# Kernel tuning notes

Hardware: AMD Instinct MI355X
Metric: run time of the kernel (lower is better)

The kernel has to match this reference:

```python
import math
import jax, jax.numpy as jnp
import numpy as np

LOG_NORM = -0.5 * math.log(2.0 * math.pi)  # per-dim gaussian normalizer
HEADS = 4
EM_ITERS = 5


def _mab(x, wq, bq, wk, bk, wv, bv, wo, bo):
    # Set-Transformer SAB(x) = MAB(x, x), ln=False
    B, S, D = x.shape
    dh = D // HEADS
    q = (x @ wq + bq).reshape(B, S, HEADS, dh)
    k = (x @ wk + bk).reshape(B, S, HEADS, dh)
    v = (x @ wv + bv).reshape(B, S, HEADS, dh)
    att = jax.nn.softmax(jnp.einsum('bqhd,bkhd->bhqk', q, k) / math.sqrt(D), axis=-1)
    o = q + jnp.einsum('bhqk,bkhd->bqhd', att, v)
    o = o.reshape(B, S, D)
    return o + jax.nn.relu(o @ wo + bo)


def setup_inputs() -> dict:
    key = jax.random.key(0)
    ks = jax.random.split(key, 16)
    B, S, D, L, K, MC = 16, 256, 512, 64, 20, 10
    s512 = 1.0 / math.sqrt(512.0)
    inp = {
        'H': jax.random.normal(ks[0], (B, S, D), jnp.float32),
        'eps': jax.random.normal(ks[1], (B * S, MC, L), jnp.float32),
        'sab_wq': jax.random.normal(ks[2], (2, D, D), jnp.float32) * s512,
        'sab_bq': jnp.zeros((2, D), jnp.float32),
        'sab_wk': jax.random.normal(ks[3], (2, D, D), jnp.float32) * s512,
        'sab_bk': jnp.zeros((2, D), jnp.float32),
        'sab_wv': jax.random.normal(ks[4], (2, D, D), jnp.float32) * s512,
        'sab_bv': jnp.zeros((2, D), jnp.float32),
        'sab_wo': jax.random.normal(ks[5], (2, D, D), jnp.float32) * s512,
        'sab_bo': jnp.zeros((2, D), jnp.float32),
        'wz': jax.random.normal(ks[6], (D, 2 * L), jnp.float32) * 0.02,
        'bz': jnp.zeros((2 * L,), jnp.float32),
        'w1': jax.random.normal(ks[7], (L, 2 * D), jnp.float32) * (1.0 / math.sqrt(L)),
        'b1': jnp.zeros((2 * D,), jnp.float32),
        'w2': jax.random.normal(ks[8], (2 * D, 2 * D), jnp.float32) * (1.0 / math.sqrt(2 * D)),
        'b2': jnp.zeros((2 * D,), jnp.float32),
        'w3': jax.random.normal(ks[9], (2 * D, D), jnp.float32) * (1.0 / math.sqrt(2 * D)),
        'b3': jnp.zeros((D,), jnp.float32),
    }
    rng = np.random.default_rng(1)
    # component_size distinct indices into the S*MC latent samples, per batch
    inp['init_idx'] = jnp.asarray(
        np.stack([rng.permutation(S * MC)[:K] for _ in range(B)]).astype(np.int32))
    return inp


def reference(H, eps, init_idx, sab_wq, sab_bq, sab_wk, sab_bk, sab_wv, sab_bv,
              sab_wo, sab_bo, wz, bz, w1, b1, w2, b2, w3, b3):
    B, S, D = H.shape
    MC, L = eps.shape[1], eps.shape[2]
    K = init_idx.shape[1]

    # q(z|x): two SABs + linear head
    h = H
    for i in range(2):
        h = _mab(h, sab_wq[i], sab_bq[i], sab_wk[i], sab_bk[i],
                 sab_wv[i], sab_bv[i], sab_wo[i], sab_bo[i])
    stats = h @ wz + bz                                    # [B,S,2L]
    mean, logvar = stats[..., :L], stats[..., L:]
    std = jnp.exp(0.5 * logvar)
    z = mean.reshape(B * S, 1, L) + eps * std.reshape(B * S, 1, L)
    z = z.reshape(B, S, MC, L)
    all_z = z.reshape(B, S * MC, L)                        # [B,N,L]

    # unsupervised EM prior (unit-variance GMM); distances via expansion
    pi = jnp.full((B, K), 1.0 / K, dtype=H.dtype)
    mu = jnp.take_along_axis(all_z, init_idx[:, :, None], axis=1)  # [B,K,L]
    x2 = jnp.sum(all_z * all_z, axis=-1)                   # [B,N]
    for _ in range(EM_ITERS):
        m2 = jnp.sum(mu * mu, axis=-1)                     # [B,K]
        ll = (-0.5 * (x2[:, :, None] - 2.0 * jnp.einsum('bnd,bkd->bnk', all_z, mu)
                      + m2[:, None, :]) + L * LOG_NORM + jnp.log(pi)[:, None, :])
        post = jax.nn.softmax(ll, axis=-1)                 # [B,N,K]
        Nk = post.sum(axis=1)                              # [B,K]
        pi = Nk / Nk.sum(axis=-1, keepdims=True)
        mu = jnp.einsum('bnk,bnd->bkd', post, all_z) / Nk[:, :, None]
    pi = jax.lax.stop_gradient(pi)
    mu = jax.lax.stop_gradient(mu)

    # reconstruction
    zf = z.reshape(-1, L)
    hr = jax.nn.relu(zf @ w1 + b1)
    hr = jax.nn.relu(hr @ w2 + b2)
    hr = jax.nn.relu(hr @ w3 + b3)
    hr = hr.reshape(B, S, MC, D)
    rec_loss = jnp.sum((hr - H[:, :, None, :]) ** 2) / (B * S * MC)

    # KL
    log_qz = jnp.sum(-0.5 * (logvar[:, :, None, :]
                             + (z - mean[:, :, None, :]) ** 2 / jnp.exp(logvar)[:, :, None, :])
                     + LOG_NORM, axis=-1)                  # [B,S,MC]
    z2 = jnp.sum(z * z, axis=-1)                           # [B,S,MC]
    m2 = jnp.sum(mu * mu, axis=-1)                         # [B,K]
    ll = (-0.5 * (z2[..., None] - 2.0 * jnp.einsum('bsmd,bkd->bsmk', z, mu)
                  + m2[:, None, None, :]) + L * LOG_NORM + jnp.log(pi)[:, None, None, :])
    log_pz = jax.scipy.special.logsumexp(ll, axis=-1)      # [B,S,MC]
    kl_loss = jnp.mean(log_qz - log_pz)
    return rec_loss, kl_loss
```

## Files before the change

kernel.cpp:

```cpp
#include <hip/hip_runtime.h>
#include <hip/hip_bf16.h>
#include <math.h>


#define BATCH 16
#define SEQ 256
#define DIM 512
#define NH 4
#define DH 128
#define LD 64
#define KC 20
#define MC 10
#define NPTS 2560
#define BS_TOT 4096
#define NROWS 40960
#define LOG_NORM (-0.9189385332046727f)

typedef __attribute__((ext_vector_type(8))) short bf16x8;
typedef __attribute__((ext_vector_type(4))) float f32x4;
typedef __hip_bfloat16 bf;

__device__ inline float warpReduceSum(float v) {
    for (int o = 32; o > 0; o >>= 1) v += __shfl_down(v, o);
    return v;
}

__device__ inline void async_copy16(const bf* g, bf* l) {
    __builtin_amdgcn_global_load_lds(
        (const __attribute__((address_space(1))) unsigned int*)g,
        (__attribute__((address_space(3))) unsigned int*)l, 16, 0, 0);
}

__device__ inline void split_store(float x, bf* ph, bf* pl, long idx) {
    const bf h = __float2bfloat16(x);
    ph[idx] = h;
    pl[idx] = __float2bfloat16(x - __bfloat162float(h));
}

template<int MODE>
__global__ __launch_bounds__(256, 3)
void gemm3t(const bf* __restrict__ Ah, const bf* __restrict__ Al,
            const bf* __restrict__ Bh, const bf* __restrict__ Bl,
            int K, int lda, int ldb,
            const float* __restrict__ b0, const float* __restrict__ b1v,
            const float* __restrict__ b2v,
            float* __restrict__ outF,
            bf* __restrict__ P1h, bf* __restrict__ P1l,
            bf* __restrict__ P2h, bf* __restrict__ P2l,
            bf* __restrict__ P3h, bf* __restrict__ P3l,
            const bf* __restrict__ Rh, const bf* __restrict__ Rl)
{
    __shared__ __align__(16) char smem[49152];
    float* Xs = (float*)smem;

    const int t = threadIdx.x;
    const int m0 = blockIdx.y * 64, n0 = blockIdx.x * 128;
    const int w = t >> 6, lane = t & 63;
    const int wn = w * 32;
    const int fm = lane & 15, quad = lane >> 4, fk = quad * 8;
    const int srow = t >> 2, scol = (t & 3) * 8;

    f32x4 acc[4][2];
#pragma unroll
    for (int i = 0; i < 4; i++)
#pragma unroll
        for (int j = 0; j < 2; j++) acc[i][j] = (f32x4){0.f, 0.f, 0.f, 0.f};

    const int nk2 = K >> 6;
    for (int kk2 = 0; kk2 < nk2; kk2++) {
#pragma unroll
        for (int h = 0; h < 2; h++) {
            const int kk = kk2 * 2 + h;
            char* base = smem + h * 24576;
            bf* Ash = (bf*)base;
            bf* Asl = (bf*)(base + 4096);
            bf* Bsh = (bf*)(base + 8192);
            bf* Bsl = (bf*)(base + 16384);
            const long ao = (long)(m0 + srow) * lda + kk * 32 + scol;
            const long bo = (long)(n0 + srow) * ldb + kk * 32 + scol;
            async_copy16(Ah + ao, Ash + w * 512);
            async_copy16(Al + ao, Asl + w * 512);
            async_copy16(Bh + bo, Bsh + w * 512);
            async_copy16(Bh + bo + 64L * ldb, Bsh + 2048 + w * 512);
            async_copy16(Bl + bo, Bsl + w * 512);
            async_copy16(Bl + bo + 64L * ldb, Bsl + 2048 + w * 512);
        }
        __syncthreads();

#pragma unroll
        for (int h = 0; h < 2; h++) {
            char* base = smem + h * 24576;
            bf* Ash = (bf*)base;
            bf* Asl = (bf*)(base + 4096);
            bf* Bsh = (bf*)(base + 8192);
            bf* Bsl = (bf*)(base + 16384);
            bf16x8 afh[4], afl[4], bfh[2], bfl[2];
#pragma unroll
            for (int mi = 0; mi < 4; mi++) {
                afh[mi] = *(const bf16x8*)&Ash[(mi * 16 + fm) * 32 + fk];
                afl[mi] = *(const bf16x8*)&Asl[(mi * 16 + fm) * 32 + fk];
            }
#pragma unroll
            for (int ni = 0; ni < 2; ni++) {
                bfh[ni] = *(const bf16x8*)&Bsh[(wn + ni * 16 + fm) * 32 + fk];
                bfl[ni] = *(const bf16x8*)&Bsl[(wn + ni * 16 + fm) * 32 + fk];
            }
#pragma unroll
            for (int mi = 0; mi < 4; mi++)
#pragma unroll
                for (int ni = 0; ni < 2; ni++) {
                    acc[mi][ni] = __builtin_amdgcn_mfma_f32_16x16x32_bf16(
                        afh[mi], bfh[ni], acc[mi][ni], 0, 0, 0);
                    acc[mi][ni] = __builtin_amdgcn_mfma_f32_16x16x32_bf16(
                        afh[mi], bfl[ni], acc[mi][ni], 0, 0, 0);
                    acc[mi][ni] = __builtin_amdgcn_mfma_f32_16x16x32_bf16(
                        afl[mi], bfh[ni], acc[mi][ni], 0, 0, 0);
                }
        }
        __syncthreads();
    }

    const int rl = t >> 2;
    const int cc4 = (t & 3) * 16;

    for (int p = 0; p < 2; p++) {
        if ((w >> 1) == p) {
            const int cb = wn - p * 64;
#pragma unroll
            for (int mi = 0; mi < 4; mi++)
#pragma unroll
                for (int ni = 0; ni < 2; ni++) {
                    const int c = cb + ni * 16 + fm;
#pragma unroll
                    for (int r = 0; r < 4; r++)
                        Xs[(mi * 16 + quad * 4 + r) * 68 + c] = acc[mi][ni][r];
                }
        }
        __syncthreads();

        if (MODE == 0 && n0 >= 1024) {
            const int hh = (n0 >> 7) & 3;
            const int dd = p * 64 + rl;
            const int bb = m0 >> 8;
            const int sb = (m0 & 255) + cc4;
            const float bias = b2v[hh * 128 + dd];
            const long ob = (((long)(bb * NH + hh) * DH + dd) << 8) + sb;
#pragma unroll
            for (int j = 0; j < 2; j++) {
                bf16x8 vh, vl;
#pragma unroll
                for (int i = 0; i < 8; i++) {
                    const float x = Xs[(cc4 + j * 8 + i) * 68 + rl] + bias;
                    const bf h = __float2bfloat16(x);
                    vh[i] = *(const short*)&h;
                    const bf l = __float2bfloat16(x - __bfloat162float(h));
                    vl[i] = *(const short*)&l;
                }
                *(bf16x8*)&P3h[ob + j * 8] = vh;
                *(bf16x8*)&P3l[ob + j * 8] = vl;
            }
        } else {
            float xv[16];
#pragma unroll
            for (int i = 0; i < 4; i++)
                *(float4*)&xv[i * 4] = *(const float4*)&Xs[rl * 68 + cc4 + i * 4];

            if (MODE == 0) {
                const int which = n0 >> 9;
                const int colq = (n0 & 511) + p * 64 + cc4;
                const float* bias = which ? b1v : b0;
                bf* Ph = which ? P2h : P1h;
                bf* Pl = which ? P2l : P1l;
                const long ob = (long)(m0 + rl) * 512 + colq;
#pragma unroll
                for (int j = 0; j < 2; j++) {
                    bf16x8 vh, vl;
#pragma unroll
                    for (int i = 0; i < 8; i++) {
                        const float x = xv[j * 8 + i] + bias[colq + j * 8 + i];
                        const bf h = __float2bfloat16(x); vh[i] = *(const short*)&h;
                        const bf l = __float2bfloat16(x - __bfloat162float(h));
                        vl[i] = *(const short*)&l;
                    }
                    *(bf16x8*)&Ph[ob + j * 8] = vh;
                    *(bf16x8*)&Pl[ob + j * 8] = vl;
                }
            } else if (MODE == 3) {
                const int colg = n0 + p * 64 + cc4;
                const long ob = (long)(m0 + rl) * 512 + colg;
#pragma unroll
                for (int j = 0; j < 2; j++) {
                    const bf16x8 rh = *(const bf16x8*)&Rh[ob + j * 8];
                    const bf16x8 rv = *(const bf16x8*)&Rl[ob + j * 8];
                    bf16x8 vh, vl;
#pragma unroll
                    for (int i = 0; i < 8; i++) {
                        short sh = rh[i], sl = rv[i];
                        float x = fmaxf(xv[j * 8 + i] + b0[colg + j * 8 + i], 0.f)
                                + __bfloat162float(*(const bf*)&sh)
                                + __bfloat162float(*(const bf*)&sl);
                        const bf h = __float2bfloat16(x); vh[i] = *(const short*)&h;
                        const bf l = __float2bfloat16(x - __bfloat162float(h));
                        vl[i] = *(const short*)&l;
                    }
                    *(bf16x8*)&P1h[ob + j * 8] = vh;
                    *(bf16x8*)&P1l[ob + j * 8] = vl;
                }
            } else {
                const int colg = p * 64 + cc4;
                const long ob = (long)(m0 + rl) * 128 + colg;
#pragma unroll
                for (int i = 0; i < 4; i++) {
                    float4 v = *(float4*)&xv[i * 4];
                    v.x += b0[colg + i * 4 + 0];
                    v.y += b0[colg + i * 4 + 1];
                    v.z += b0[colg + i * 4 + 2];
                    v.w += b0[colg + i * 4 + 3];
                    *(float4*)&outF[ob + i * 4] = v;
                }
            }
        }
        __syncthreads();
    }
}

__global__ __launch_bounds__(256)
void attn_fused(const bf* __restrict__ qh, const bf* __restrict__ ql,
                const bf* __restrict__ kh, const bf* __restrict__ kl,
                const bf* __restrict__ vTh, const bf* __restrict__ vTl,
                bf* __restrict__ oh, bf* __restrict__ ol)
{
    __shared__ __align__(16) char smem[43008];
    bf* Qsh = (bf*)smem;            bf* Qsl = (bf*)(smem + 4096);
    bf* Ksh = (bf*)(smem + 8192);   bf* Ksl = (bf*)(smem + 24576);
    bf* Psh = (bf*)smem;            bf* Psl = (bf*)(smem + 4096);
    bf* Vsh = (bf*)(smem + 8192);   bf* Vsl = (bf*)(smem + 16384);
    float (*red)[4]  = (float(*)[4])(smem + 40960);
    float (*red2)[4] = (float(*)[4])(smem + 41984);

    const int t = threadIdx.x;
    const int z = blockIdx.y;
    const int m0 = blockIdx.x * 64;
    const int bb = z >> 2, hh = z & 3;
    const long hOff = (long)bb * 131072 + (long)hh * 128;
    const long vOff = (long)z * 32768;

    const int w = t >> 6, lane = t & 63;
    const int fm = lane & 15;
    const int quad = lane >> 4;
    const int fk = quad * 8;
    const int srow = t >> 2, scol = (t & 3) * 8;

    f32x4 acc[4][4];
#pragma unroll
    for (int i = 0; i < 4; i++)
#pragma unroll
        for (int j = 0; j < 4; j++) acc[i][j] = (f32x4){0.f, 0.f, 0.f, 0.f};

    for (int kk = 0; kk < 4; kk++) {
        const long ao = hOff + (long)(m0 + srow) * 512 + kk * 32 + scol;
        const long bo = hOff + (long)srow * 512 + kk * 32 + scol;
        async_copy16(qh + ao, Qsh + w * 512);
        async_copy16(ql + ao, Qsl + w * 512);
#pragma unroll
        for (int j = 0; j < 4; j++) {
            async_copy16(kh + bo + (long)j * 64 * 512, Ksh + w * 512 + j * 2048);
            async_copy16(kl + bo + (long)j * 64 * 512, Ksl + w * 512 + j * 2048);
        }
        __syncthreads();

        bf16x8 afh[4], afl[4];
#pragma unroll
        for (int mi = 0; mi < 4; mi++) {
            afh[mi] = *(const bf16x8*)&Qsh[(mi * 16 + fm) * 32 + fk];
            afl[mi] = *(const bf16x8*)&Qsl[(mi * 16 + fm) * 32 + fk];
        }
#pragma unroll
        for (int ni = 0; ni < 4; ni++) {
            const bf16x8 bh = *(const bf16x8*)&Ksh[(w * 64 + ni * 16 + fm) * 32 + fk];
            const bf16x8 bl = *(const bf16x8*)&Ksl[(w * 64 + ni * 16 + fm) * 32 + fk];
#pragma unroll
            for (int mi = 0; mi < 4; mi++) {
                acc[mi][ni] = __builtin_amdgcn_mfma_f32_16x16x32_bf16(
                    afh[mi], bh, acc[mi][ni], 0, 0, 0);
                acc[mi][ni] = __builtin_amdgcn_mfma_f32_16x16x32_bf16(
                    afh[mi], bl, acc[mi][ni], 0, 0, 0);
                acc[mi][ni] = __builtin_amdgcn_mfma_f32_16x16x32_bf16(
                    afl[mi], bh, acc[mi][ni], 0, 0, 0);
            }
        }
        __syncthreads();
    }

    const float alpha = 0.044194173824159216f;
#pragma unroll
    for (int mi = 0; mi < 4; mi++)
#pragma unroll
        for (int r = 0; r < 4; r++) {
            float m = -1e30f;
#pragma unroll
            for (int ni = 0; ni < 4; ni++) m = fmaxf(m, acc[mi][ni][r]);
            for (int o = 8; o > 0; o >>= 1) m = fmaxf(m, __shfl_xor(m, o));
            if (fm == 0) red[mi * 16 + quad * 4 + r][w] = m;
        }
    __syncthreads();
    float invr[4][4];
#pragma unroll
    for (int mi = 0; mi < 4; mi++)
#pragma unroll
        for (int r = 0; r < 4; r++) {
            const int rowl = mi * 16 + quad * 4 + r;
            const float mx = fmaxf(fmaxf(red[rowl][0], red[rowl][1]),
                                   fmaxf(red[rowl][2], red[rowl][3]));
            float s = 0.f;
#pragma unroll
            for (int ni = 0; ni < 4; ni++) {
                const float e = __expf((acc[mi][ni][r] - mx) * alpha);
                acc[mi][ni][r] = e;
                s += e;
            }
            for (int o = 8; o > 0; o >>= 1) s += __shfl_xor(s, o);
            if (fm == 0) red2[rowl][w] = s;
        }
    __syncthreads();
#pragma unroll
    for (int mi = 0; mi < 4; mi++)
#pragma unroll
        for (int r = 0; r < 4; r++) {
            const int rowl = mi * 16 + quad * 4 + r;
            invr[mi][r] = 1.f / (red2[rowl][0] + red2[rowl][1] + red2[rowl][2] + red2[rowl][3]);
        }

    f32x4 acc2[4][2];
#pragma unroll
    for (int i = 0; i < 4; i++)
#pragma unroll
        for (int j = 0; j < 2; j++) acc2[i][j] = (f32x4){0.f, 0.f, 0.f, 0.f};

    for (int kc = 0; kc < 8; kc++) {
        if (w == (kc >> 1)) {
            const int nib = (kc & 1) * 2;
#pragma unroll
            for (int mi = 0; mi < 4; mi++)
#pragma unroll
                for (int r = 0; r < 4; r++) {
                    const int row = mi * 16 + quad * 4 + r;
#pragma unroll
                    for (int j = 0; j < 2; j++) {
                        const float p = acc[mi][nib + j][r] * invr[mi][r];
                        const int cc = j * 16 + fm;
                        const bf h = __float2bfloat16(p);
                        Psh[row * 32 + cc] = h;
                        Psl[row * 32 + cc] = __float2bfloat16(p - __bfloat162float(h));
                    }
                }
        }
        const long vo = vOff + (long)srow * 256 + kc * 32 + scol;
        async_copy16(vTh + vo, Vsh + w * 512);
        async_copy16(vTh + vo + 64L * 256, Vsh + w * 512 + 2048);
        async_copy16(vTl + vo, Vsl + w * 512);
        async_copy16(vTl + vo + 64L * 256, Vsl + w * 512 + 2048);
        __syncthreads();

        bf16x8 pfh[4], pfl[4];
#pragma unroll
        for (int mi = 0; mi < 4; mi++) {
            pfh[mi] = *(const bf16x8*)&Psh[(mi * 16 + fm) * 32 + fk];
            pfl[mi] = *(const bf16x8*)&Psl[(mi * 16 + fm) * 32 + fk];
        }
#pragma unroll
        for (int ni = 0; ni < 2; ni++) {
            const bf16x8 vh = *(const bf16x8*)&Vsh[(w * 32 + ni * 16 + fm) * 32 + fk];
            const bf16x8 vl = *(const bf16x8*)&Vsl[(w * 32 + ni * 16 + fm) * 32 + fk];
#pragma unroll
            for (int mi = 0; mi < 4; mi++) {
                acc2[mi][ni] = __builtin_amdgcn_mfma_f32_16x16x32_bf16(
                    pfh[mi], vh, acc2[mi][ni], 0, 0, 0);
                acc2[mi][ni] = __builtin_amdgcn_mfma_f32_16x16x32_bf16(
                    pfh[mi], vl, acc2[mi][ni], 0, 0, 0);
                acc2[mi][ni] = __builtin_amdgcn_mfma_f32_16x16x32_bf16(
                    pfl[mi], vh, acc2[mi][ni], 0, 0, 0);
            }
        }
        __syncthreads();
    }

#pragma unroll
    for (int ni = 0; ni < 2; ni++) {
        const int col = hh * 128 + w * 32 + ni * 16 + fm;
#pragma unroll
        for (int mi = 0; mi < 4; mi++)
#pragma unroll
            for (int r = 0; r < 4; r++) {
                const int row = mi * 16 + quad * 4 + r;
                const long idx = (long)(bb * 256 + m0 + row) * 512 + col;
                const float x = acc2[mi][ni][r]
                    + __bfloat162float(qh[idx]) + __bfloat162float(ql[idx]);
                split_store(x, oh, ol, idx);
            }
    }
}

template<bool SQLOSS>
__global__ __launch_bounds__(256, 4)
void gemm_mfma(const bf* __restrict__ A, const bf* __restrict__ BT,
               bf* __restrict__ C,
               const float* __restrict__ bias,
               const float* __restrict__ Href,
               float* __restrict__ lossAcc,
               int K, int N)
{
    __shared__ __align__(16) char smem[32768];
    bf* Cs  = (bf*)smem;
    __shared__ float redS[4];

    const int t = threadIdx.x;
    const int flat = blockIdx.y * gridDim.x + blockIdx.x;
    const int lane8 = flat & 7;
    const int grp = flat >> 3;
    const int n_blk = grp % gridDim.x;
    const int m_blk = (grp / gridDim.x) * 8 + lane8;
    const int m0 = m_blk * 128, n0 = n_blk * 128;

    const int w = t >> 6, lane = t & 63;
    const int wm = (w >> 1) * 64, wn = (w & 1) * 64;
    const int fm = lane & 15;
    const int quad = lane >> 4;
    const int fk = quad * 8;
    const int srow = t >> 2, scol = (t & 3) * 8;

    f32x4 acc[4][4];
#pragma unroll
    for (int i = 0; i < 4; i++)
#pragma unroll
        for (int j = 0; j < 4; j++) acc[i][j] = (f32x4){0.f, 0.f, 0.f, 0.f};

    const int nk2 = K >> 6;
    for (int kt2 = 0; kt2 < nk2; kt2++) {
#pragma unroll
        for (int h = 0; h < 2; h++) {
            const int kt = kt2 * 2 + h;
            bf* Asg = (bf*)(smem + h * 16384);
            bf* Bsg = (bf*)(smem + h * 16384 + 8192);
            const bf* ga = A + (long)(m0 + srow) * K + kt * 32 + scol;
            const bf* gb = BT + (long)(n0 + srow) * K + kt * 32 + scol;
            async_copy16(ga, Asg + w * 512);
            async_copy16(ga + 64L * K, Asg + 2048 + w * 512);
            async_copy16(gb, Bsg + w * 512);
            async_copy16(gb + 64L * K, Bsg + 2048 + w * 512);
        }
        __syncthreads();

#pragma unroll
        for (int h = 0; h < 2; h++) {
            bf* Asg = (bf*)(smem + h * 16384);
            bf* Bsg = (bf*)(smem + h * 16384 + 8192);
            bf16x8 af[4], bfr[4];
#pragma unroll
            for (int mi = 0; mi < 4; mi++)
                af[mi] = *(const bf16x8*)&Asg[(wm + mi * 16 + fm) * 32 + fk];
#pragma unroll
            for (int ni = 0; ni < 4; ni++)
                bfr[ni] = *(const bf16x8*)&Bsg[(wn + ni * 16 + fm) * 32 + fk];
#pragma unroll
            for (int mi = 0; mi < 4; mi++)
#pragma unroll
                for (int ni = 0; ni < 4; ni++)
                    acc[mi][ni] = __builtin_amdgcn_mfma_f32_16x16x32_bf16(
                        af[mi], bfr[ni], acc[mi][ni], 0, 0, 0);
        }
        __syncthreads();
    }

    if (SQLOSS) {
        float lsum = 0.f;
#pragma unroll
        for (int ni = 0; ni < 4; ni++) {
            const int col = n0 + wn + ni * 16 + fm;
            const float b = bias[col];
#pragma unroll
            for (int mi = 0; mi < 4; mi++)
#pragma unroll
                for (int r = 0; r < 4; r++) {
                    const int row = m0 + wm + mi * 16 + quad * 4 + r;
                    const float x = fmaxf(acc[mi][ni][r] + b, 0.f);
                    const float d = x - Href[(long)(row / MC) * DIM + col];
                    lsum = fmaf(d, d, lsum);
                }
        }
        lsum = warpReduceSum(lsum);
        if (lane == 0) redS[w] = lsum;
        __syncthreads();
        if (t == 0) atomicAdd(lossAcc, redS[0] + redS[1] + redS[2] + redS[3]);
    } else {
        for (int hf = 0; hf < 2; hf++) {
            if ((w >> 1) == hf) {
#pragma unroll
                for (int ni = 0; ni < 4; ni++) {
                    const int c = wn + ni * 16 + fm;
                    const float bv = bias[n0 + c];
#pragma unroll
                    for (int mi = 0; mi < 4; mi++)
#pragma unroll
                        for (int r = 0; r < 4; r++) {
                            const float x = fmaxf(acc[mi][ni][r] + bv, 0.f);
                            Cs[(mi * 16 + quad * 4 + r) * 136 + c] = __float2bfloat16(x);
                        }
                }
            }
            __syncthreads();
            const int rl2 = t >> 2, cc2 = (t & 3) * 32;
            const long ob = (long)(m0 + hf * 64 + rl2) * N + n0 + cc2;
#pragma unroll
            for (int j = 0; j < 4; j++)
                *(bf16x8*)&C[ob + j * 8] = *(const bf16x8*)&Cs[rl2 * 136 + cc2 + j * 8];
            __syncthreads();
        }
    }
}

__global__ void conv_all(
    const float* __restrict__ H, bf* __restrict__ h0h, bf* __restrict__ h0l,
    const float* __restrict__ wq, const float* __restrict__ wk,
    const float* __restrict__ wv, const float* __restrict__ wo,
    bf* __restrict__ qkvTh0, bf* __restrict__ qkvTl0,
    bf* __restrict__ woTh0, bf* __restrict__ woTl0,
    bf* __restrict__ qkvTh1, bf* __restrict__ qkvTl1,
    bf* __restrict__ woTh1, bf* __restrict__ woTl1,
    const float* __restrict__ wz, bf* __restrict__ wzTh, bf* __restrict__ wzTl,
    const float* __restrict__ w1, bf* __restrict__ w1T,
    const float* __restrict__ w2, bf* __restrict__ w2T,
    const float* __restrict__ w3, bf* __restrict__ w3T,
    float* __restrict__ scal, float* __restrict__ msP, float* __restrict__ nkP)
{
    const int t = threadIdx.x;
    if (blockIdx.x == 0 && t < 16) scal[t] = 0.f;
    const int gidx = blockIdx.x * 256 + t;
    if (gidx < 2097152) {
        const float x = H[gidx];
        const bf h = __float2bfloat16(x);
        h0h[gidx] = h;
        h0l[gidx] = __float2bfloat16(x - __bfloat162float(h));
        return;
    }
    const int idx = gidx - 2097152;
    if (idx < 2097152) {
        const int layer = idx >> 20;
        const int seg = (idx >> 18) & 3;
        const int r = idx & 262143;
        const int k = r >> 9, n = r & 511;
        const float* src = ((seg == 0) ? wq : (seg == 1) ? wk : (seg == 2) ? wv : wo)
                           + (long)layer * 262144;
        const float x = src[r];
        const bf h = __float2bfloat16(x);
        const bf l = __float2bfloat16(x - __bfloat162float(h));
        if (seg < 3) {
            const long o = (long)(seg * 512 + n) * 512 + k;
            if (layer == 0) { qkvTh0[o] = h; qkvTl0[o] = l; }
            else            { qkvTh1[o] = h; qkvTl1[o] = l; }
        } else {
            const long o = (long)n * 512 + k;
            if (layer == 0) { woTh0[o] = h; woTl0[o] = l; }
            else            { woTh1[o] = h; woTl1[o] = l; }
        }
    } else if (idx < 2162688) {
        const int i = idx - 2097152;
        const int k = i >> 7, n = i & 127;
        const float x = wz[i];
        const bf h = __float2bfloat16(x);
        wzTh[(long)n * 512 + k] = h;
        wzTl[(long)n * 512 + k] = __float2bfloat16(x - __bfloat162float(h));
    } else if (idx < 2228224) {
        const int i = idx - 2162688;
        const int k = i >> 10, n = i & 1023;
        w1T[(long)n * 64 + k] = __float2bfloat16(w1[i]);
    } else if (idx < 3276800) {
        const int i = idx - 2228224;
        const int k = i >> 10, n = i & 1023;
        w2T[(long)n * 1024 + k] = __float2bfloat16(w2[i]);
    } else if (idx < 3801088) {
        const int i = idx - 3276800;
        const int k = i >> 9, n = i & 511;
        w3T[(long)n * 1024 + k] = __float2bfloat16(w3[i]);
    } else if (idx < 3903488) {
        msP[20480 + (idx - 3801088)] = 0.f;
    } else if (idx < 3905088) {
        nkP[320 + (idx - 3903488)] = 0.f;
    }
}

__global__ __launch_bounds__(256)
void zgen(const float* __restrict__ stats, const float* __restrict__ eps,
          float* __restrict__ z, bf* __restrict__ z16)
{
    const int idx = blockIdx.x * 256 + threadIdx.x;
    const int bs = idx / 160;
    const int r = idx % 160;
    const int l4 = r % 16;
    const float4 e = ((const float4*)eps)[idx];
    const float4 mn = ((const float4*)stats)[bs * 32 + l4];
    const float4 lv = ((const float4*)stats)[bs * 32 + 16 + l4];
    float4 zz;
    zz.x = fmaf(e.x, expf(0.5f * lv.x), mn.x);
    zz.y = fmaf(e.y, expf(0.5f * lv.y), mn.y);
    zz.z = fmaf(e.z, expf(0.5f * lv.z), mn.z);
    zz.w = fmaf(e.w, expf(0.5f * lv.w), mn.w);
    ((float4*)z)[idx] = zz;
    bf* zp = z16 + (long)idx * 4;
    zp[0] = __float2bfloat16(zz.x);
    zp[1] = __float2bfloat16(zz.y);
    zp[2] = __float2bfloat16(zz.z);
    zp[3] = __float2bfloat16(zz.w);
}

__global__ void em_init(const float* __restrict__ z, const int* __restrict__ init_idx,
                        float* __restrict__ ms0, float* __restrict__ nk0)
{
    const int b = blockIdx.x, t = threadIdx.x;
    for (int i = t; i < KC * LD; i += 256) {
        const int k = i >> 6, l = i & 63;
        const int idx = init_idx[b * KC + k];
        ms0[b * KC * LD + i] = z[((long)b * NPTS + idx) * LD + l];
    }
    if (t < KC) nk0[b * KC + t] = 1.f;
}

__global__ __launch_bounds__(256)
void em_step(const float* __restrict__ z,
             const float* __restrict__ msIn, const float* __restrict__ nkIn,
             float* __restrict__ msOut, float* __restrict__ nkOut)
{
    __shared__ float muS[KC][65];
    __shared__ float m2lp[KC];
    __shared__ float NkU[KC];
    __shared__ float postS[KC][256];
    __shared__ float NkS[KC];

    const int tile = blockIdx.x, b = blockIdx.y, t = threadIdx.x;
    const int lane = t & 63, w = t >> 6;

    if (t < KC) NkU[t] = nkIn[b * KC + t];
    __syncthreads();
    for (int i = t; i < KC * LD; i += 256)
        muS[i >> 6][i & 63] = msIn[b * KC * LD + i] / NkU[i >> 6];
    __syncthreads();
    if (t < KC) {
        float s = 0.f;
        for (int l = 0; l < LD; l++) { const float m = muS[t][l]; s = fmaf(m, m, s); }
        float sn = 0.f;
        for (int k = 0; k < KC; k++) sn += NkU[k];
        m2lp[t] = -0.5f * s + logf(NkU[t] / sn);
    }
    __syncthreads();

    const long n = (long)tile * 256 + t;
    const float* zr = &z[((long)b * NPTS + n) * LD];
    float acc[KC];
#pragma unroll
    for (int k = 0; k < KC; k++) acc[k] = 0.f;
#pragma unroll
    for (int l4 = 0; l4 < 16; l4++) {
        const float4 zv = ((const float4*)zr)[l4];
#pragma unroll
        for (int k = 0; k < KC; k++) {
            acc[k] = fmaf(zv.x, muS[k][l4 * 4 + 0], acc[k]);
            acc[k] = fmaf(zv.y, muS[k][l4 * 4 + 1], acc[k]);
            acc[k] = fmaf(zv.z, muS[k][l4 * 4 + 2], acc[k]);
            acc[k] = fmaf(zv.w, muS[k][l4 * 4 + 3], acc[k]);
        }
    }
    float mx = -1e30f;
    float llv[KC];
#pragma unroll
    for (int k = 0; k < KC; k++) { llv[k] = acc[k] + m2lp[k]; mx = fmaxf(mx, llv[k]); }
    float s = 0.f;
#pragma unroll
    for (int k = 0; k < KC; k++) { llv[k] = expf(llv[k] - mx); s += llv[k]; }
    const float inv = 1.f / s;
#pragma unroll
    for (int k = 0; k < KC; k++) postS[k][t] = llv[k] * inv;
    __syncthreads();

#pragma unroll
    for (int kk = 0; kk < 5; kk++) {
        const int k = w * 5 + kk;
        float p = postS[k][lane] + postS[k][lane + 64] + postS[k][lane + 128] + postS[k][lane + 192];
        p = warpReduceSum(p);
        if (lane == 0) NkS[k] = p;
    }
    __syncthreads();

    const float* zb = &z[((long)b * NPTS + (long)tile * 256) * LD];
#pragma unroll
    for (int j = 0; j < 5; j++) {
        const int o = t + j * 256;
        const int k = o >> 6, l = o & 63;
        float sacc = 0.f;
        for (int n2 = 0; n2 < 256; n2++)
            sacc = fmaf(postS[k][n2], zb[n2 * LD + l], sacc);
        atomicAdd(&msOut[b * KC * LD + o], sacc);
    }
    if (t < KC) atomicAdd(&nkOut[b * KC + t], NkS[t]);
}

__global__ __launch_bounds__(256)
void kl_kernel(const float* __restrict__ z, const float* __restrict__ stats,
               const float* __restrict__ eps,
               const float* __restrict__ msIn, const float* __restrict__ nkIn,
               float* __restrict__ klAcc)
{
    __shared__ float muS[KC][65];
    __shared__ float m2lp[KC];
    __shared__ float NkU[KC];
    __shared__ float redS[4];

    const int tile = blockIdx.x, b = blockIdx.y, t = threadIdx.x;

    if (t < KC) NkU[t] = nkIn[b * KC + t];
    __syncthreads();
    for (int i = t; i < KC * LD; i += 256)
        muS[i >> 6][i & 63] = msIn[b * KC * LD + i] / NkU[i >> 6];
    __syncthreads();
    if (t < KC) {
        float s = 0.f;
        for (int l = 0; l < LD; l++) { const float m = muS[t][l]; s = fmaf(m, m, s); }
        float sn = 0.f;
        for (int k = 0; k < KC; k++) sn += NkU[k];
        m2lp[t] = -0.5f * s + logf(NkU[t] / sn);
    }
    __syncthreads();

    const int n = tile * 256 + t;
    const int sidx = n / MC, m = n % MC;
    const long bs = (long)b * SEQ + sidx;
    const float* zr = &z[((long)b * NPTS + n) * LD];

    float acc[KC];
#pragma unroll
    for (int k = 0; k < KC; k++) acc[k] = 0.f;
    float x2 = 0.f;
#pragma unroll
    for (int l4 = 0; l4 < 16; l4++) {
        const float4 zv = ((const float4*)zr)[l4];
        x2 = fmaf(zv.x, zv.x, fmaf(zv.y, zv.y, fmaf(zv.z, zv.z, fmaf(zv.w, zv.w, x2))));
#pragma unroll
        for (int k = 0; k < KC; k++) {
            acc[k] = fmaf(zv.x, muS[k][l4 * 4 + 0], acc[k]);
            acc[k] = fmaf(zv.y, muS[k][l4 * 4 + 1], acc[k]);
            acc[k] = fmaf(zv.z, muS[k][l4 * 4 + 2], acc[k]);
            acc[k] = fmaf(zv.w, muS[k][l4 * 4 + 3], acc[k]);
        }
    }
    float mx = -1e30f;
    float llv[KC];
#pragma unroll
    for (int k = 0; k < KC; k++) { llv[k] = acc[k] + m2lp[k]; mx = fmaxf(mx, llv[k]); }
    float s = 0.f;
#pragma unroll
    for (int k = 0; k < KC; k++) s += expf(llv[k] - mx);
    const float log_pz = -0.5f * x2 + mx + logf(s) + LD * LOG_NORM;

    const float* lvr = &stats[bs * 128 + 64];
    const float* er = &eps[(bs * MC + m) * LD];
    float slv = 0.f, se2 = 0.f;
#pragma unroll
    for (int l4 = 0; l4 < 16; l4++) {
        const float4 lv = ((const float4*)lvr)[l4];
        slv += lv.x + lv.y + lv.z + lv.w;
        const float4 e = ((const float4*)er)[l4];
        se2 = fmaf(e.x, e.x, fmaf(e.y, e.y, fmaf(e.z, e.z, fmaf(e.w, e.w, se2))));
    }
    const float log_qz = -0.5f * (slv + se2) + LD * LOG_NORM;

    float v = log_qz - log_pz;
    v = warpReduceSum(v);
    if ((t & 63) == 0) redS[t >> 6] = v;
    __syncthreads();
    if (t == 0) atomicAdd(klAcc, redS[0] + redS[1] + redS[2] + redS[3]);
}

__global__ void finalize(const float* __restrict__ scal, float* __restrict__ out)
{
    if (threadIdx.x == 0) {
        out[0] = scal[0] * (1.f / (float)NROWS);
        out[1] = scal[1] * (1.f / (float)NROWS);
    }
}

extern "C" void kernel_launch(void* const* d_in, const int* in_sizes, int n_in,
                              void* d_out, int out_size, void* d_ws, size_t ws_size,
                              hipStream_t stream)
{
    const float* H   = (const float*)d_in[0];
    const float* eps = (const float*)d_in[1];
    const float* wq  = (const float*)d_in[2];
    const float* bq  = (const float*)d_in[3];
    const float* wk  = (const float*)d_in[4];
    const float* bk  = (const float*)d_in[5];
    const float* wv  = (const float*)d_in[6];
    const float* bv  = (const float*)d_in[7];
    const float* wo  = (const float*)d_in[8];
    const float* bo  = (const float*)d_in[9];
    const float* wz  = (const float*)d_in[10];
    const float* bz  = (const float*)d_in[11];
    const float* w1  = (const float*)d_in[12];
    const float* b1  = (const float*)d_in[13];
    const float* w2  = (const float*)d_in[14];
    const float* b2  = (const float*)d_in[15];
    const float* w3  = (const float*)d_in[16];
    const float* b3  = (const float*)d_in[17];
    const int* init_idx = (const int*)d_in[18];
    float* out = (float*)d_out;
    float* wsf = (float*)d_ws;

    const long o_scal  = 0;
    const long o_nk    = 1024;
    const long o_ms    = 4096;
    const long o_st    = 131072;
    const long o_zb    = 655360;
    const long o_z16   = 3276800;
    const long o_q     = 4587520;
    const long o_k     = 6684672;
    const long o_vT    = 8781824;
    const long o_o     = 10878976;
    const long o_h1    = 12976128;
    const long o_qkvT0 = 15073280;
    const long o_woT0  = 15859712;
    const long o_qkvT1 = 16121856;
    const long o_woT1  = 16908288;
    const long o_wzT   = 17170432;
    const long o_w1T   = 17235968;
    const long o_w2T   = 17268736;
    const long o_w3T   = 17793024;
    const long o_d1    = 18055168;
    const long o_d2    = 39026688;

    const long PL = (long)BS_TOT * DIM;
    bf* qh  = (bf*)(wsf + o_q);   bf* ql  = qh + PL;
    bf* kh  = (bf*)(wsf + o_k);   bf* kl_ = kh + PL;
    bf* vTh = (bf*)(wsf + o_vT);  bf* vTl = vTh + PL;
    bf* oh  = (bf*)(wsf + o_o);   bf* ol  = oh + PL;
    bf* h1h = (bf*)(wsf + o_h1);  bf* h1l = h1h + PL;
    bf* h2h = qh;                 bf* h2l = ql;
    bf* qkvTh0 = (bf*)(wsf + o_qkvT0); bf* qkvTl0 = qkvTh0 + 1536L * 512;
    bf* woTh0  = (bf*)(wsf + o_woT0);  bf* woTl0  = woTh0 + 512L * 512;
    bf* qkvTh1 = (bf*)(wsf + o_qkvT1); bf* qkvTl1 = qkvTh1 + 1536L * 512;
    bf* woTh1  = (bf*)(wsf + o_woT1);  bf* woTl1  = woTh1 + 512L * 512;
    bf* wzTh = (bf*)(wsf + o_wzT);     bf* wzTl = wzTh + 128L * 512;
    bf* w1T = (bf*)(wsf + o_w1T);
    bf* w2T = (bf*)(wsf + o_w2T);
    bf* w3T = (bf*)(wsf + o_w3T);
    bf* z16 = (bf*)(wsf + o_z16);
    bf* d1  = (bf*)(wsf + o_d1);
    bf* d2  = (bf*)(wsf + o_d2);
    float* st = wsf + o_st;
    float* zb = wsf + o_zb;
    float* scal = wsf + o_scal;
    float* msP = wsf + o_ms;
    float* nkP = wsf + o_nk;

    const dim3 blk(256);

    conv_all<<<23447, blk, 0, stream>>>(
        H, h1h, h1l,
        wq, wk, wv, wo,
        qkvTh0, qkvTl0, woTh0, woTl0,
        qkvTh1, qkvTl1, woTh1, woTl1,
        wz, wzTh, wzTl, w1, w1T, w2, w2T, w3, w3T,
        scal, msP, nkP);

    for (int i = 0; i < 2; i++) {
        const long boff = (long)i * DIM;
        bf* qkh = i ? qkvTh1 : qkvTh0;  bf* qkl = i ? qkvTl1 : qkvTl0;
        bf* wh  = i ? woTh1 : woTh0;    bf* wl  = i ? woTl1 : woTl0;

        gemm3t<0><<<dim3(12, 64), blk, 0, stream>>>(
            h1h, h1l, qkh, qkl, 512, 512, 512,
            bq + boff, bk + boff, bv + boff, nullptr,
            qh, ql, kh, kl_, vTh, vTl, nullptr, nullptr);
        attn_fused<<<dim3(4, 64), blk, 0, stream>>>(qh, ql, kh, kl_, vTh, vTl, oh, ol);
        bf* houth = (i == 0) ? h1h : h2h;
        bf* houtl = (i == 0) ? h1l : h2l;
        gemm3t<3><<<dim3(4, 64), blk, 0, stream>>>(
            oh, ol, wh, wl, 512, 512, 512,
            bo + boff, nullptr, nullptr, nullptr,
            houth, houtl, nullptr, nullptr, nullptr, nullptr, oh, ol);
    }

    gemm3t<4><<<dim3(1, 64), blk, 0, stream>>>(
        h2h, h2l, wzTh, wzTl, 512, 512, 512,
        bz, nullptr, nullptr, st,
        nullptr, nullptr, nullptr, nullptr, nullptr, nullptr, nullptr, nullptr);

    zgen<<<2560, blk, 0, stream>>>(st, eps, zb, z16);

    gemm_mfma<false><<<dim3(8, 320), blk, 0, stream>>>(
        z16, w1T, d1, b1, nullptr, nullptr, 64, 1024);
    gemm_mfma<false><<<dim3(8, 320), blk, 0, stream>>>(
        d1, w2T, d2, b2, nullptr, nullptr, 1024, 1024);
    gemm_mfma<true><<<dim3(4, 320), blk, 0, stream>>>(
        d2, w3T, nullptr, b3, H, scal + 0, 1024, 512);

    em_init<<<16, blk, 0, stream>>>(zb, init_idx, msP, nkP);
    for (int it = 0; it < 5; it++) {
        em_step<<<dim3(10, 16), blk, 0, stream>>>(
            zb,
            msP + (long)it * 16 * KC * LD, nkP + (long)it * 16 * KC,
            msP + (long)(it + 1) * 16 * KC * LD, nkP + (long)(it + 1) * 16 * KC);
    }
    kl_kernel<<<dim3(10, 16), blk, 0, stream>>>(
        zb, st, eps,
        msP + 5L * 16 * KC * LD, nkP + 5L * 16 * KC, scal + 1);

    finalize<<<1, 64, 0, stream>>>(scal, out);
}
```

Measured before the change: 687.3 us.

## Fuse EM iterations, KL and finalize into one persistent kernel with grid barrier

Replaces em_init, the five em_step launches, kl_kernel and finalize with a single persistent kernel of 160 blocks. A software grid barrier built on device-scope atomics replaces the kernel boundaries between steps. The initial means are read directly from z at init_idx, and the barrier counters are zeroed in conv_all. This removes about seven launch gaps in exchange for spin-wait barrier latency, and it relies on all 160 blocks being resident at the same time.

```diff
diff --git a/kernel.cpp b/kernel.cpp
--- a/kernel.cpp
+++ b/kernel.cpp
@@ -35,6 +35,27 @@
     const bf h = __float2bfloat16(x);
     ph[idx] = h;
     pl[idx] = __float2bfloat16(x - __bfloat162float(h));
+}
+
+__device__ inline void gbar(unsigned* cnt, unsigned* gen, unsigned nblk) {
+    __syncthreads();
+    if (threadIdx.x == 0) {
+        const unsigned g = __hip_atomic_load(gen, __ATOMIC_ACQUIRE,
+                                             __HIP_MEMORY_SCOPE_AGENT);
+        const unsigned a = __hip_atomic_fetch_add(cnt, 1u, __ATOMIC_ACQ_REL,
+                                                  __HIP_MEMORY_SCOPE_AGENT);
+        if (a + 1u == nblk) {
+            __hip_atomic_store(cnt, 0u, __ATOMIC_RELAXED,
+                               __HIP_MEMORY_SCOPE_AGENT);
+            __hip_atomic_store(gen, g + 1u, __ATOMIC_RELEASE,
+                               __HIP_MEMORY_SCOPE_AGENT);
+        } else {
+            while (__hip_atomic_load(gen, __ATOMIC_ACQUIRE,
+                                     __HIP_MEMORY_SCOPE_AGENT) == g)
+                __builtin_amdgcn_s_sleep(2);
+        }
+    }
+    __syncthreads();
 }
 
 template<int MODE>
@@ -535,6 +556,8 @@
 {
     const int t = threadIdx.x;
     if (blockIdx.x == 0 && t < 16) scal[t] = 0.f;
+    if (blockIdx.x == 0 && t >= 16 && t < 24)
+        ((unsigned*)scal)[496 + t] = 0u;
     const int gidx = blockIdx.x * 256 + t;
     if (gidx < 2097152) {
         const float x = H[gidx];
@@ -613,177 +636,193 @@
     zp[3] = __float2bfloat16(zz.w);
 }
 
-__global__ void em_init(const float* __restrict__ z, const int* __restrict__ init_idx,
-                        float* __restrict__ ms0, float* __restrict__ nk0)
-{
-    const int b = blockIdx.x, t = threadIdx.x;
-    for (int i = t; i < KC * LD; i += 256) {
-        const int k = i >> 6, l = i & 63;
-        const int idx = init_idx[b * KC + k];
-        ms0[b * KC * LD + i] = z[((long)b * NPTS + idx) * LD + l];
-    }
-    if (t < KC) nk0[b * KC + t] = 1.f;
-}
-
 __global__ __launch_bounds__(256)
-void em_step(const float* __restrict__ z,
-             const float* __restrict__ msIn, const float* __restrict__ nkIn,
-             float* __restrict__ msOut, float* __restrict__ nkOut)
+void em_all(const float* __restrict__ z, const int* __restrict__ init_idx,
+            const float* __restrict__ stats, const float* __restrict__ eps,
+            float* __restrict__ msP, float* __restrict__ nkP,
+            float* __restrict__ scal, float* __restrict__ out,
+            unsigned* __restrict__ bar)
 {
     __shared__ float muS[KC][65];
     __shared__ float m2lp[KC];
     __shared__ float NkU[KC];
     __shared__ float postS[KC][256];
     __shared__ float NkS[KC];
+    __shared__ float redS[4];
 
     const int tile = blockIdx.x, b = blockIdx.y, t = threadIdx.x;
     const int lane = t & 63, w = t >> 6;
-
-    if (t < KC) NkU[t] = nkIn[b * KC + t];
-    __syncthreads();
-    for (int i = t; i < KC * LD; i += 256)
-        muS[i >> 6][i & 63] = msIn[b * KC * LD + i] / NkU[i >> 6];
-    __syncthreads();
-    if (t < KC) {
+    const unsigned NBLK = 160u;
+
+    for (int it = 0; it < 5; it++) {
+        if (it == 0) {
+            if (t < KC) NkU[t] = 1.f;
+            __syncthreads();
+            for (int i = t; i < KC * LD; i += 256) {
+                const int k = i >> 6, l = i & 63;
+                const int idx = init_idx[b * KC + k];
+                muS[k][l] = z[((long)b * NPTS + idx) * LD + l];
+            }
+        } else {
+            const float* msIn = msP + (long)it * 16 * KC * LD;
+            const float* nkIn = nkP + (long)it * 16 * KC;
+            if (t < KC)
+                NkU[t] = __hip_atomic_load(&nkIn[b * KC + t],
+                                           __ATOMIC_RELAXED,
+                                           __HIP_MEMORY_SCOPE_AGENT);
+            __syncthreads();
+            for (int i = t; i < KC * LD; i += 256)
+                muS[i >> 6][i & 63] =
+                    __hip_atomic_load(&msIn[b * KC * LD + i],
+                                      __ATOMIC_RELAXED,
+                                      __HIP_MEMORY_SCOPE_AGENT) / NkU[i >> 6];
+        }
+        __syncthreads();
+        if (t < KC) {
+            float s = 0.f;
+            for (int l = 0; l < LD; l++) { const float m = muS[t][l]; s = fmaf(m, m, s); }
+            float sn = 0.f;
+            for (int k = 0; k < KC; k++) sn += NkU[k];
+            m2lp[t] = -0.5f * s + logf(NkU[t] / sn);
+        }
+        __syncthreads();
+
+        const long n = (long)tile * 256 + t;
+        const float* zr = &z[((long)b * NPTS + n) * LD];
+        float acc[KC];
+#pragma unroll
+        for (int k = 0; k < KC; k++) acc[k] = 0.f;
+#pragma unroll
+        for (int l4 = 0; l4 < 16; l4++) {
+            const float4 zv = ((const float4*)zr)[l4];
+#pragma unroll
+            for (int k = 0; k < KC; k++) {
+                acc[k] = fmaf(zv.x, muS[k][l4 * 4 + 0], acc[k]);
+                acc[k] = fmaf(zv.y, muS[k][l4 * 4 + 1], acc[k]);
+                acc[k] = fmaf(zv.z, muS[k][l4 * 4 + 2], acc[k]);
+                acc[k] = fmaf(zv.w, muS[k][l4 * 4 + 3], acc[k]);
+            }
+        }
+        float mx = -1e30f;
+        float llv[KC];
+#pragma unroll
+        for (int k = 0; k < KC; k++) { llv[k] = acc[k] + m2lp[k]; mx = fmaxf(mx, llv[k]); }
         float s = 0.f;
-        for (int l = 0; l < LD; l++) { const float m = muS[t][l]; s = fmaf(m, m, s); }
-        float sn = 0.f;
-        for (int k = 0; k < KC; k++) sn += NkU[k];
-        m2lp[t] = -0.5f * s + logf(NkU[t] / sn);
-    }
-    __syncthreads();
-
-    const long n = (long)tile * 256 + t;
-    const float* zr = &z[((long)b * NPTS + n) * LD];
-    float acc[KC];
-#pragma unroll
-    for (int k = 0; k < KC; k++) acc[k] = 0.f;
-#pragma unroll
-    for (int l4 = 0; l4 < 16; l4++) {
-        const float4 zv = ((const float4*)zr)[l4];
-#pragma unroll
-        for (int k = 0; k < KC; k++) {
-            acc[k] = fmaf(zv.x, muS[k][l4 * 4 + 0], acc[k]);
-            acc[k] = fmaf(zv.y, muS[k][l4 * 4 + 1], acc[k]);
-            acc[k] = fmaf(zv.z, muS[k][l4 * 4 + 2], acc[k]);
-            acc[k] = fmaf(zv.w, muS[k][l4 * 4 + 3], acc[k]);
-        }
-    }
-    float mx = -1e30f;
-    float llv[KC];
-#pragma unroll
-    for (int k = 0; k < KC; k++) { llv[k] = acc[k] + m2lp[k]; mx = fmaxf(mx, llv[k]); }
-    float s = 0.f;
-#pragma unroll
-    for (int k = 0; k < KC; k++) { llv[k] = expf(llv[k] - mx); s += llv[k]; }
-    const float inv = 1.f / s;
-#pragma unroll
-    for (int k = 0; k < KC; k++) postS[k][t] = llv[k] * inv;
-    __syncthreads();
-
-#pragma unroll
-    for (int kk = 0; kk < 5; kk++) {
-        const int k = w * 5 + kk;
-        float p = postS[k][lane] + postS[k][lane + 64] + postS[k][lane + 128] + postS[k][lane + 192];
-        p = warpReduceSum(p);
-        if (lane == 0) NkS[k] = p;
-    }
-    __syncthreads();
-
-    const float* zb = &z[((long)b * NPTS + (long)tile * 256) * LD];
-#pragma unroll
-    for (int j = 0; j < 5; j++) {
-        const int o = t + j * 256;
-        const int k = o >> 6, l = o & 63;
-        float sacc = 0.f;
-        for (int n2 = 0; n2 < 256; n2++)
-            sacc = fmaf(postS[k][n2], zb[n2 * LD + l], sacc);
-        atomicAdd(&msOut[b * KC * LD + o], sacc);
-    }
-    if (t < KC) atomicAdd(&nkOut[b * KC + t], NkS[t]);
-}
-
-__global__ __launch_bounds__(256)
-void kl_kernel(const float* __restrict__ z, const float* __restrict__ stats,
-               const float* __restrict__ eps,
-               const float* __restrict__ msIn, const float* __restrict__ nkIn,
-               float* __restrict__ klAcc)
-{
-    __shared__ float muS[KC][65];
-    __shared__ float m2lp[KC];
-    __shared__ float NkU[KC];
-    __shared__ float redS[4];
-
-    const int tile = blockIdx.x, b = blockIdx.y, t = threadIdx.x;
-
-    if (t < KC) NkU[t] = nkIn[b * KC + t];
-    __syncthreads();
-    for (int i = t; i < KC * LD; i += 256)
-        muS[i >> 6][i & 63] = msIn[b * KC * LD + i] / NkU[i >> 6];
-    __syncthreads();
-    if (t < KC) {
+#pragma unroll
+        for (int k = 0; k < KC; k++) { llv[k] = expf(llv[k] - mx); s += llv[k]; }
+        const float inv = 1.f / s;
+#pragma unroll
+        for (int k = 0; k < KC; k++) postS[k][t] = llv[k] * inv;
+        __syncthreads();
+
+#pragma unroll
+        for (int kk = 0; kk < 5; kk++) {
+            const int k = w * 5 + kk;
+            float p = postS[k][lane] + postS[k][lane + 64]
+                    + postS[k][lane + 128] + postS[k][lane + 192];
+            p = warpReduceSum(p);
+            if (lane == 0) NkS[k] = p;
+        }
+        __syncthreads();
+
+        float* msOut = msP + (long)(it + 1) * 16 * KC * LD;
+        float* nkOut = nkP + (long)(it + 1) * 16 * KC;
+        const float* zb = &z[((long)b * NPTS + (long)tile * 256) * LD];
+#pragma unroll
+        for (int j = 0; j < 5; j++) {
+            const int o = t + j * 256;
+            const int k = o >> 6, l = o & 63;
+            float sacc = 0.f;
+            for (int n2 = 0; n2 < 256; n2++)
+                sacc = fmaf(postS[k][n2], zb[n2 * LD + l], sacc);
+            atomicAdd(&msOut[b * KC * LD + o], sacc);
+        }
+        if (t < KC) atomicAdd(&nkOut[b * KC + t], NkS[t]);
+
+        gbar(bar, bar + 1, NBLK);
+    }
+
+    {
+        const float* msIn = msP + 5L * 16 * KC * LD;
+        const float* nkIn = nkP + 5L * 16 * KC;
+        if (t < KC)
+            NkU[t] = __hip_atomic_load(&nkIn[b * KC + t],
+                                       __ATOMIC_RELAXED,
+                                       __HIP_MEMORY_SCOPE_AGENT);
+        __syncthreads();
+        for (int i = t; i < KC * LD; i += 256)
+            muS[i >> 6][i & 63] =
+                __hip_atomic_load(&msIn[b * KC * LD + i],
+                                  __ATOMIC_RELAXED,
+                                  __HIP_MEMORY_SCOPE_AGENT) / NkU[i >> 6];
+        __syncthreads();
+        if (t < KC) {
+            float s = 0.f;
+            for (int l = 0; l < LD; l++) { const float m = muS[t][l]; s = fmaf(m, m, s); }
+            float sn = 0.f;
+            for (int k = 0; k < KC; k++) sn += NkU[k];
+            m2lp[t] = -0.5f * s + logf(NkU[t] / sn);
+        }
+        __syncthreads();
+
+        const int n = tile * 256 + t;
+        const int sidx = n / MC, m = n % MC;
+        const long bs = (long)b * SEQ + sidx;
+        const float* zr = &z[((long)b * NPTS + n) * LD];
+
+        float acc[KC];
+#pragma unroll
+        for (int k = 0; k < KC; k++) acc[k] = 0.f;
+        float x2 = 0.f;
+#pragma unroll
+        for (int l4 = 0; l4 < 16; l4++) {
+            const float4 zv = ((const float4*)zr)[l4];
+            x2 = fmaf(zv.x, zv.x, fmaf(zv.y, zv.y, fmaf(zv.z, zv.z, fmaf(zv.w, zv.w, x2))));
+#pragma unroll
+            for (int k = 0; k < KC; k++) {
+                acc[k] = fmaf(zv.x, muS[k][l4 * 4 + 0], acc[k]);
+                acc[k] = fmaf(zv.y, muS[k][l4 * 4 + 1], acc[k]);
+                acc[k] = fmaf(zv.z, muS[k][l4 * 4 + 2], acc[k]);
+                acc[k] = fmaf(zv.w, muS[k][l4 * 4 + 3], acc[k]);
+            }
+        }
+        float mx = -1e30f;
+        float llv[KC];
+#pragma unroll
+        for (int k = 0; k < KC; k++) { llv[k] = acc[k] + m2lp[k]; mx = fmaxf(mx, llv[k]); }
         float s = 0.f;
-        for (int l = 0; l < LD; l++) { const float m = muS[t][l]; s = fmaf(m, m, s); }
-        float sn = 0.f;
-        for (int k = 0; k < KC; k++) sn += NkU[k];
-        m2lp[t] = -0.5f * s + logf(NkU[t] / sn);
-    }
-    __syncthreads();
-
-    const int n = tile * 256 + t;
-    const int sidx = n / MC, m = n % MC;
-    const long bs = (long)b * SEQ + sidx;
-    const float* zr = &z[((long)b * NPTS + n) * LD];
-
-    float acc[KC];
-#pragma unroll
-    for (int k = 0; k < KC; k++) acc[k] = 0.f;
-    float x2 = 0.f;
-#pragma unroll
-    for (int l4 = 0; l4 < 16; l4++) {
-        const float4 zv = ((const float4*)zr)[l4];
-        x2 = fmaf(zv.x, zv.x, fmaf(zv.y, zv.y, fmaf(zv.z, zv.z, fmaf(zv.w, zv.w, x2))));
-#pragma unroll
-        for (int k = 0; k < KC; k++) {
-            acc[k] = fmaf(zv.x, muS[k][l4 * 4 + 0], acc[k]);
-            acc[k] = fmaf(zv.y, muS[k][l4 * 4 + 1], acc[k]);
-            acc[k] = fmaf(zv.z, muS[k][l4 * 4 + 2], acc[k]);
-            acc[k] = fmaf(zv.w, muS[k][l4 * 4 + 3], acc[k]);
-        }
-    }
-    float mx = -1e30f;
-    float llv[KC];
-#pragma unroll
-    for (int k = 0; k < KC; k++) { llv[k] = acc[k] + m2lp[k]; mx = fmaxf(mx, llv[k]); }
-    float s = 0.f;
-#pragma unroll
-    for (int k = 0; k < KC; k++) s += expf(llv[k] - mx);
-    const float log_pz = -0.5f * x2 + mx + logf(s) + LD * LOG_NORM;
-
-    const float* lvr = &stats[bs * 128 + 64];
-    const float* er = &eps[(bs * MC + m) * LD];
-    float slv = 0.f, se2 = 0.f;
-#pragma unroll
-    for (int l4 = 0; l4 < 16; l4++) {
-        const float4 lv = ((const float4*)lvr)[l4];
-        slv += lv.x + lv.y + lv.z + lv.w;
-        const float4 e = ((const float4*)er)[l4];
-        se2 = fmaf(e.x, e.x, fmaf(e.y, e.y, fmaf(e.z, e.z, fmaf(e.w, e.w, se2))));
-    }
-    const float log_qz = -0.5f * (slv + se2) + LD * LOG_NORM;
-
-    float v = log_qz - log_pz;
-    v = warpReduceSum(v);
-    if ((t & 63) == 0) redS[t >> 6] = v;
-    __syncthreads();
-    if (t == 0) atomicAdd(klAcc, redS[0] + redS[1] + redS[2] + redS[3]);
-}
-
-__global__ void finalize(const float* __restrict__ scal, float* __restrict__ out)
-{
-    if (threadIdx.x == 0) {
-        out[0] = scal[0] * (1.f / (float)NROWS);
-        out[1] = scal[1] * (1.f / (float)NROWS);
+#pragma unroll
+        for (int k = 0; k < KC; k++) s += expf(llv[k] - mx);
+        const float log_pz = -0.5f * x2 + mx + logf(s) + LD * LOG_NORM;
+
+        const float* lvr = &stats[bs * 128 + 64];
+        const float* er = &eps[(bs * MC + m) * LD];
+        float slv = 0.f, se2 = 0.f;
+#pragma unroll
+        for (int l4 = 0; l4 < 16; l4++) {
+            const float4 lv = ((const float4*)lvr)[l4];
+            slv += lv.x + lv.y + lv.z + lv.w;
+            const float4 e = ((const float4*)er)[l4];
+            se2 = fmaf(e.x, e.x, fmaf(e.y, e.y, fmaf(e.z, e.z, fmaf(e.w, e.w, se2))));
+        }
+        const float log_qz = -0.5f * (slv + se2) + LD * LOG_NORM;
+
+        float v = log_qz - log_pz;
+        v = warpReduceSum(v);
+        if ((t & 63) == 0) redS[t >> 6] = v;
+        __syncthreads();
+        if (t == 0) atomicAdd(&scal[1], redS[0] + redS[1] + redS[2] + redS[3]);
+    }
+
+    gbar(bar, bar + 1, NBLK);
+
+    if (tile == 0 && b == 0 && t == 0) {
+        const float r0 = __hip_atomic_load(&scal[0], __ATOMIC_RELAXED,
+                                           __HIP_MEMORY_SCOPE_AGENT);
+        const float k1 = __hip_atomic_load(&scal[1], __ATOMIC_RELAXED,
+                                           __HIP_MEMORY_SCOPE_AGENT);
+        out[0] = r0 * (1.f / (float)NROWS);
+        out[1] = k1 * (1.f / (float)NROWS);
     }
 }
 
@@ -858,6 +897,7 @@
     float* scal = wsf + o_scal;
     float* msP = wsf + o_ms;
     float* nkP = wsf + o_nk;
+    unsigned* bar = (unsigned*)(wsf) + 512;
 
     const dim3 blk(256);
 
@@ -901,16 +941,6 @@
     gemm_mfma<true><<<dim3(4, 320), blk, 0, stream>>>(
         d2, w3T, nullptr, b3, H, scal + 0, 1024, 512);
 
-    em_init<<<16, blk, 0, stream>>>(zb, init_idx, msP, nkP);
-    for (int it = 0; it < 5; it++) {
-        em_step<<<dim3(10, 16), blk, 0, stream>>>(
-            zb,
-            msP + (long)it * 16 * KC * LD, nkP + (long)it * 16 * KC,
-            msP + (long)(it + 1) * 16 * KC * LD, nkP + (long)(it + 1) * 16 * KC);
-    }
-    kl_kernel<<<dim3(10, 16), blk, 0, stream>>>(
-        zb, st, eps,
-        msP + 5L * 16 * KC * LD, nkP + 5L * 16 * KC, scal + 1);
-
-    finalize<<<1, 64, 0, stream>>>(scal, out);
-}
+    em_all<<<dim3(10, 16), blk, 0, stream>>>(
+        zb, init_idx, st, eps, msP, nkP, scal, out, bar);
+}
```

After: 822.2 us. +19.6%, slower.
